# Kernel optimization log

Measured on AMD Instinct MI355X. Metric: run time of the kernel, lower is better.

Reference implementation:

```python
import jax, jax.numpy as jnp
import numpy as np

MASK_VALUE = float(-2**32 + 1)  # additive fill used by the torch module
B, QT, KT, D = 16, 2048, 2048, 1024


def setup_inputs() -> dict:
    key = jax.random.key(0)
    kq, kk, kv, kql, kkl = jax.random.split(key, 5)
    return {
        "Q": jax.random.normal(kq, (B, QT, D), dtype=jnp.float32),
        "K": jax.random.normal(kk, (B, KT, D), dtype=jnp.float32),
        "V": jax.random.normal(kv, (B, KT, D), dtype=jnp.float32),
        "Q_lengths": jax.random.randint(kql, (B,), 1, QT + 1, dtype=jnp.int32),
        "K_lengths": jax.random.randint(kkl, (B,), 1, KT + 1, dtype=jnp.int32),
    }


def reference(Q, K, V, Q_lengths, K_lengths):
    # dot-product scores: [b, qt, kt]
    logits = jnp.einsum("bqd,bkd->bqk", Q, K)
    # length mask: outer product of row-valid and col-valid masks
    q_valid = (jnp.arange(Q.shape[1]) < Q_lengths[:, None]).astype(logits.dtype)  # [b, qt]
    k_valid = (jnp.arange(K.shape[1]) < K_lengths[:, None]).astype(logits.dtype)  # [b, kt]
    mask = q_valid[:, :, None] * k_valid[:, None, :]                               # [b, qt, kt]
    logits = mask * logits + (1.0 - mask) * MASK_VALUE
    attention = jax.nn.softmax(logits, axis=-1)
    return jnp.einsum("bqk,bkd->bqd", attention, V)
```

## Files before the change

### kernel.cpp

```cpp
#include <hip/hip_runtime.h>

#define BATCH 16
#define QT    2048
#define KTOT  2048
#define DIM   1024
#define NITEMS (BATCH * (QT / 32))

typedef __attribute__((ext_vector_type(8))) _Float16 f16x8;
typedef __attribute__((ext_vector_type(4))) _Float16 f16x4;
typedef __attribute__((ext_vector_type(2))) _Float16 f16x2;
typedef __attribute__((ext_vector_type(4))) float    f32x4;

__global__ __launch_bounds__(256) void conv_k(const float* __restrict__ K,
                                              _Float16* __restrict__ Kf) {
    const size_t idx = ((size_t)blockIdx.x * 256 + threadIdx.x) * 8;
    f32x4 a0 = *(const f32x4*)(K + idx);
    f32x4 a1 = *(const f32x4*)(K + idx + 4);
    f16x8 h;
#pragma unroll
    for (int j = 0; j < 4; ++j) { h[j] = (_Float16)a0[j]; h[4 + j] = (_Float16)a1[j]; }
    *(f16x8*)(Kf + idx) = h;
}

__global__ __launch_bounds__(256) void trans_v(const float* __restrict__ V,
                                               _Float16* __restrict__ Vt) {
    const int blk = blockIdx.x;
    const int b   = blk >> 9;
    const int kt0 = ((blk >> 4) & 31) << 6;
    const int d0  = (blk & 15) << 6;
    __shared__ _Float16 tbuf[64][65];
    const int tid = threadIdx.x;
    const int cr  = tid >> 4;
    const int c4  = (tid & 15) << 2;
#pragma unroll
    for (int p = 0; p < 4; ++p) {
        const int r = cr + p * 16;
        f32x4 v = *(const f32x4*)(V + ((size_t)(b * KTOT + kt0 + r)) * DIM + d0 + c4);
#pragma unroll
        for (int j = 0; j < 4; ++j) tbuf[r][c4 + j] = (_Float16)v[j];
    }
    __syncthreads();
#pragma unroll
    for (int p = 0; p < 4; ++p) {
        const int dr = cr + p * 16;
        f16x4 o;
#pragma unroll
        for (int j = 0; j < 4; ++j) o[j] = tbuf[c4 + j][dr];
        *(f16x4*)(Vt + ((size_t)(b * DIM + d0 + dr)) * KTOT + kt0 + c4) = o;
    }
}

__global__ __launch_bounds__(64) void fill_mean_vt(const _Float16* __restrict__ Vt,
                                                   const int* __restrict__ Qlen,
                                                   float* __restrict__ out) {
    const int row = blockIdx.x * 64 + threadIdx.x;
    const int b = row >> 10, d = row & 1023;
    const f16x8* src = (const f16x8*)(Vt + (size_t)row * KTOT);
    float s = 0.0f;
    for (int i = 0; i < KTOT / 8; ++i) {
        f16x8 v = src[i];
#pragma unroll
        for (int j = 0; j < 8; ++j) s += (float)v[j];
    }
    const float mv = s * (1.0f / (float)KTOT);
    const int qlen = Qlen[b];
    for (int q = qlen; q < QT; ++q)
        out[((size_t)(b * QT + q)) * DIM + d] = mv;
}

__global__ __launch_bounds__(512, 2) void attn_main(
    const float* __restrict__ Q, const int* __restrict__ Qlen, const int* __restrict__ Klen,
    const _Float16* __restrict__ Kf, const _Float16* __restrict__ Vt,
    float* __restrict__ out, unsigned* __restrict__ counter) {

    __shared__ float    sred[2][8][32][33];
    __shared__ _Float16 pbuf[2][32][40];
    __shared__ float    arow[2][32];
    __shared__ float    lrow[32];
    __shared__ unsigned item_s;

    const int tid  = threadIdx.x;
    const int w    = tid >> 6;
    const int ln   = tid & 63;
    const int l16  = ln & 15;
    const int quad = ln >> 4;
    const int d0   = w << 7;
    const int sr  = tid >> 4;
    const int scg = tid & 15;

    for (;;) {
        __syncthreads();
        if (tid == 0) item_s = atomicAdd(counter, 1u);
        __syncthreads();
        const unsigned item = item_s;
        if (item >= NITEMS) break;
        const int b    = item >> 6;
        const int qt   = (item & 63) << 5;
        const int qlen = Qlen[b];
        if (qt >= qlen) continue;
        const int klen = Klen[b];
        const int nkt  = (klen + 31) >> 5;

        f16x8 qh[2][4], ql[2][4];
#pragma unroll
        for (int mi = 0; mi < 2; ++mi)
#pragma unroll
            for (int kc = 0; kc < 4; ++kc) {
                const float* src = Q + ((size_t)(b * QT + qt + mi * 16 + l16)) * DIM
                                     + d0 + kc * 32 + quad * 8;
                f32x4 a0 = *(const f32x4*)src;
                f32x4 a1 = *(const f32x4*)(src + 4);
                f16x8 h, l;
#pragma unroll
                for (int j = 0; j < 4; ++j) {
                    _Float16 h0 = (_Float16)a0[j];
                    h[j] = h0; l[j] = (_Float16)(a0[j] - (float)h0);
                    _Float16 h1 = (_Float16)a1[j];
                    h[4 + j] = h1; l[4 + j] = (_Float16)(a1[j] - (float)h1);
                }
                qh[mi][kc] = h; ql[mi][kc] = l;
            }

        f32x4 o[2][8];
        const f32x4 fzero = {0.0f, 0.0f, 0.0f, 0.0f};
#pragma unroll
        for (int mi = 0; mi < 2; ++mi)
#pragma unroll
            for (int nd = 0; nd < 8; ++nd) o[mi][nd] = fzero;

        float msx = -3.0e38f, lsx = 0.0f;

        f16x8 kf[2][4];
        {
            const _Float16* kb = Kf + ((size_t)(b * KTOT + l16)) * DIM + d0 + quad * 8;
#pragma unroll
            for (int ni = 0; ni < 2; ++ni)
#pragma unroll
                for (int kc = 0; kc < 4; ++kc)
                    kf[ni][kc] = *(const f16x8*)(kb + (size_t)(ni * 16) * DIM + kc * 32);
        }

        f16x8 vf[8];

        for (int t = 0; t <= nkt; ++t) {
            const int cur = t & 1, prv = cur ^ 1;

            if (t < nkt) {
                f32x4 s[2][2];
                s[0][0] = fzero; s[0][1] = fzero; s[1][0] = fzero; s[1][1] = fzero;
#pragma unroll
                for (int kc = 0; kc < 4; ++kc)
#pragma unroll
                    for (int ni = 0; ni < 2; ++ni) {
                        s[0][ni] = __builtin_amdgcn_mfma_f32_16x16x32_f16(qh[0][kc], kf[ni][kc], s[0][ni], 0, 0, 0);
                        s[1][ni] = __builtin_amdgcn_mfma_f32_16x16x32_f16(qh[1][kc], kf[ni][kc], s[1][ni], 0, 0, 0);
                        s[0][ni] = __builtin_amdgcn_mfma_f32_16x16x32_f16(ql[0][kc], kf[ni][kc], s[0][ni], 0, 0, 0);
                        s[1][ni] = __builtin_amdgcn_mfma_f32_16x16x32_f16(ql[1][kc], kf[ni][kc], s[1][ni], 0, 0, 0);
                    }
#pragma unroll
                for (int mi = 0; mi < 2; ++mi)
#pragma unroll
                    for (int ni = 0; ni < 2; ++ni)
#pragma unroll
                        for (int r2 = 0; r2 < 4; ++r2)
                            sred[cur][w][mi * 16 + quad * 4 + r2][ni * 16 + l16] = s[mi][ni][r2];
            }

            if (t > 0) {
                const int kt0p = (t - 1) << 5;
                const int c0 = scg * 2, c1 = c0 + 1;
                float x0 = 0.0f, x1 = 0.0f;
#pragma unroll
                for (int ww = 0; ww < 8; ++ww) {
                    x0 += sred[prv][ww][sr][c0];
                    x1 += sred[prv][ww][sr][c1];
                }
                if (kt0p + c0 >= klen) x0 = -3.0e38f;
                if (kt0p + c1 >= klen) x1 = -3.0e38f;
                float pm = fmaxf(x0, x1);
#pragma unroll
                for (int off = 1; off < 16; off <<= 1) pm = fmaxf(pm, __shfl_xor(pm, off, 64));
                const float mn    = fmaxf(msx, pm);
                const float alpha = __expf(msx - mn);
                const float p0 = __expf(x0 - mn), p1 = __expf(x1 - mn);
                float ps = p0 + p1;
#pragma unroll
                for (int off = 1; off < 16; off <<= 1) ps += __shfl_xor(ps, off, 64);
                lsx = lsx * alpha + ps;
                msx = mn;
                f16x2 pw; pw[0] = (_Float16)p0; pw[1] = (_Float16)p1;
                *(f16x2*)&pbuf[prv][sr][c0] = pw;
                if (scg == 0) arow[prv][sr] = alpha;
            }

            if (t + 1 < nkt) {
                const int ktn = (t + 1) << 5;
                const _Float16* kb = Kf + ((size_t)(b * KTOT + ktn + l16)) * DIM
                                        + d0 + quad * 8;
#pragma unroll
                for (int ni = 0; ni < 2; ++ni)
#pragma unroll
                    for (int kc = 0; kc < 4; ++kc)
                        kf[ni][kc] = *(const f16x8*)(kb + (size_t)(ni * 16) * DIM + kc * 32);
            }

            __syncthreads();

            if (t > 0) {
                f32x4 av0 = *(const f32x4*)&arow[prv][quad * 4];
                f32x4 av1 = *(const f32x4*)&arow[prv][16 + quad * 4];
#pragma unroll
                for (int nd = 0; nd < 8; ++nd) { o[0][nd] *= av0; o[1][nd] *= av1; }

                f16x8 pa[2];
#pragma unroll
                for (int mi = 0; mi < 2; ++mi)
                    pa[mi] = *(const f16x8*)&pbuf[prv][mi * 16 + l16][quad * 8];
#pragma unroll
                for (int nd = 0; nd < 8; ++nd) {
                    o[0][nd] = __builtin_amdgcn_mfma_f32_16x16x32_f16(pa[0], vf[nd], o[0][nd], 0, 0, 0);
                    o[1][nd] = __builtin_amdgcn_mfma_f32_16x16x32_f16(pa[1], vf[nd], o[1][nd], 0, 0, 0);
                }
            }

            if (t < nkt) {
                const int kt0 = t << 5;
#pragma unroll
                for (int nd = 0; nd < 8; ++nd)
                    vf[nd] = *(const f16x8*)(Vt + ((size_t)(b * DIM + d0 + nd * 16 + l16)) * KTOT
                                             + kt0 + quad * 8);
            }
        }

        if (scg == 0) lrow[sr] = lsx;
        __syncthreads();
        f32x4 li0, li1;
#pragma unroll
        for (int r2 = 0; r2 < 4; ++r2) {
            li0[r2] = 1.0f / lrow[quad * 4 + r2];
            li1[r2] = 1.0f / lrow[16 + quad * 4 + r2];
        }
#pragma unroll
        for (int mi = 0; mi < 2; ++mi)
#pragma unroll
            for (int r2 = 0; r2 < 4; ++r2) {
                const int row = qt + mi * 16 + quad * 4 + r2;
                if (row < qlen) {
                    const float inv = mi ? li1[r2] : li0[r2];
#pragma unroll
                    for (int nd = 0; nd < 8; ++nd)
                        out[((size_t)(b * QT + row)) * DIM + d0 + nd * 16 + l16] =
                            o[mi][nd][r2] * inv;
                }
            }
    }
}

__global__ __launch_bounds__(256) void fill_mean_f32(const float* __restrict__ V,
                                                     const int* __restrict__ Qlen,
                                                     float* __restrict__ out) {
    const int b  = blockIdx.x >> 4;
    const int d0 = (blockIdx.x & 15) << 6;
    const int qlen = Qlen[b];
    const int tid = threadIdx.x;
    const int dc = d0 + (tid & 63);
    const int part = tid >> 6;
    __shared__ float red[4][64];
    __shared__ float mcol[64];
    float sm = 0.0f;
    for (int kt = part; kt < KTOT; kt += 4)
        sm += V[((size_t)(b * KTOT + kt)) * DIM + dc];
    red[part][tid & 63] = sm;
    __syncthreads();
    if (tid < 64)
        mcol[tid] = (red[0][tid] + red[1][tid] + red[2][tid] + red[3][tid]) * (1.0f / (float)KTOT);
    __syncthreads();
    const float mv = mcol[tid & 63];
    for (int q = qlen + part; q < QT; q += 4)
        out[((size_t)(b * QT + q)) * DIM + dc] = mv;
}

__global__ __launch_bounds__(512) void attn_naive(
    const float* __restrict__ Q, const float* __restrict__ K, const float* __restrict__ V,
    const int* __restrict__ Qlen, const int* __restrict__ Klen, float* __restrict__ out) {
    const int blk  = blockIdx.x;
    const int b    = blk >> 8;
    const int qb   = (blk & 255) << 3;
    const int qlen = Qlen[b];
    if (qb >= qlen) return;
    const int klen = Klen[b];
    const int tid  = threadIdx.x;
    const int wid  = tid >> 6, ln = tid & 63;
    const int q    = qb + wid;
    __shared__ float kbuf[1024], vbuf[1024];
    f32x4 qr[4];
#pragma unroll
    for (int i = 0; i < 4; ++i)
        qr[i] = *(const f32x4*)(Q + ((size_t)(b * QT + q)) * DIM + i * 256 + ln * 4);
    const f32x4 fzero = {0.0f, 0.0f, 0.0f, 0.0f};
    f32x4 acc[4] = {fzero, fzero, fzero, fzero};
    float m = -3.0e38f, l = 0.0f;
    for (int kt = 0; kt < klen; ++kt) {
        __syncthreads();
        if (tid < 256)
            *(f32x4*)&kbuf[tid * 4] = *(const f32x4*)(K + ((size_t)(b * KTOT + kt)) * DIM + tid * 4);
        else
            *(f32x4*)&vbuf[(tid - 256) * 4] =
                *(const f32x4*)(V + ((size_t)(b * KTOT + kt)) * DIM + (tid - 256) * 4);
        __syncthreads();
        float sp = 0.0f;
#pragma unroll
        for (int i = 0; i < 4; ++i) {
            f32x4 kv = *(const f32x4*)&kbuf[i * 256 + ln * 4];
            sp += qr[i][0] * kv[0] + qr[i][1] * kv[1] + qr[i][2] * kv[2] + qr[i][3] * kv[3];
        }
#pragma unroll
        for (int off = 1; off < 64; off <<= 1) sp += __shfl_xor(sp, off, 64);
        const float mn = fmaxf(m, sp);
        const float a  = __expf(m - mn);
        const float p  = __expf(sp - mn);
        l = l * a + p; m = mn;
#pragma unroll
        for (int i = 0; i < 4; ++i) {
            f32x4 vv = *(const f32x4*)&vbuf[i * 256 + ln * 4];
            acc[i] = acc[i] * a + vv * p;
        }
    }
    if (q < qlen) {
        const float inv = 1.0f / l;
#pragma unroll
        for (int i = 0; i < 4; ++i)
            *(f32x4*)(out + ((size_t)(b * QT + q)) * DIM + i * 256 + ln * 4) = acc[i] * inv;
    }
}

extern "C" void kernel_launch(void* const* d_in, const int* in_sizes, int n_in,
                              void* d_out, int out_size, void* d_ws, size_t ws_size,
                              hipStream_t stream) {
    (void)in_sizes; (void)n_in; (void)out_size;
    const float* Q    = (const float*)d_in[0];
    const float* K    = (const float*)d_in[1];
    const float* V    = (const float*)d_in[2];
    const int*   Qlen = (const int*)d_in[3];
    const int*   Klen = (const int*)d_in[4];
    float*       out  = (float*)d_out;

    const size_t HALF = (size_t)BATCH * KTOT * DIM;
    const size_t NEED = HALF * 2  * sizeof(_Float16) + 64;
    if (ws_size >= NEED) {
        _Float16* kf = (_Float16*)d_ws;
        _Float16* vt = kf + HALF;
        unsigned* ctr = (unsigned*)((char*)d_ws + HALF * 2 * sizeof(_Float16));
        hipMemsetAsync(ctr, 0, sizeof(unsigned), stream);
        conv_k<<<dim3(16384), dim3(256), 0, stream>>>(K, kf);
        trans_v<<<dim3(8192), dim3(256), 0, stream>>>(V, vt);
        fill_mean_vt<<<dim3((BATCH * DIM) / 64), dim3(64), 0, stream>>>(vt, Qlen, out);
        attn_main<<<dim3(512), dim3(512), 0, stream>>>(Q, Qlen, Klen, kf, vt, out, ctr);
    } else {
        fill_mean_f32<<<dim3(BATCH * 16), dim3(256), 0, stream>>>(V, Qlen, out);
        attn_naive<<<dim3(4096), dim3(512), 0, stream>>>(Q, K, V, Qlen, Klen, out);
    }
}
```

Measured before the change: 781.3 us.

## Double-buffer K fragments two tiles ahead and parallelize mean fill kernel

The main attention loop is unrolled by two with two K register buffers, so each K tile is loaded two iterations before use instead of one, giving more latency hiding at the cost of extra registers. The score reduction buffer row is padded to 34 so pairs of scores can be read as float2. The fill-mean kernel splits each row sum across four threads with shuffle reduction and strides the output writes, and the persistent attention grid is halved to 256 blocks. Higher register pressure could reduce occupancy, and the smaller grid may leave compute units idle.

```diff
diff --git a/kernel.cpp b/kernel.cpp
--- a/kernel.cpp
+++ b/kernel.cpp
@@ -10,6 +10,7 @@
 typedef __attribute__((ext_vector_type(4))) _Float16 f16x4;
 typedef __attribute__((ext_vector_type(2))) _Float16 f16x2;
 typedef __attribute__((ext_vector_type(4))) float    f32x4;
+typedef __attribute__((ext_vector_type(2))) float    f32x2;
 
 __global__ __launch_bounds__(256) void conv_k(const float* __restrict__ K,
                                               _Float16* __restrict__ Kf) {
@@ -50,21 +51,25 @@
     }
 }
 
-__global__ __launch_bounds__(64) void fill_mean_vt(const _Float16* __restrict__ Vt,
-                                                   const int* __restrict__ Qlen,
-                                                   float* __restrict__ out) {
-    const int row = blockIdx.x * 64 + threadIdx.x;
+__global__ __launch_bounds__(256) void fill_mean_vt(const _Float16* __restrict__ Vt,
+                                                    const int* __restrict__ Qlen,
+                                                    float* __restrict__ out) {
+    const int gid  = blockIdx.x * 256 + threadIdx.x;
+    const int row  = gid >> 2;
+    const int part = gid & 3;
     const int b = row >> 10, d = row & 1023;
-    const f16x8* src = (const f16x8*)(Vt + (size_t)row * KTOT);
+    const f16x8* src = (const f16x8*)(Vt + (size_t)row * KTOT) + part * (KTOT / 32);
     float s = 0.0f;
-    for (int i = 0; i < KTOT / 8; ++i) {
+    for (int i = 0; i < KTOT / 32; ++i) {
         f16x8 v = src[i];
 #pragma unroll
         for (int j = 0; j < 8; ++j) s += (float)v[j];
     }
+    s += __shfl_xor(s, 1, 64);
+    s += __shfl_xor(s, 2, 64);
     const float mv = s * (1.0f / (float)KTOT);
     const int qlen = Qlen[b];
-    for (int q = qlen; q < QT; ++q)
+    for (int q = qlen + part; q < QT; q += 4)
         out[((size_t)(b * QT + q)) * DIM + d] = mv;
 }
 
@@ -73,7 +78,7 @@
     const _Float16* __restrict__ Kf, const _Float16* __restrict__ Vt,
     float* __restrict__ out, unsigned* __restrict__ counter) {
 
-    __shared__ float    sred[2][8][32][33];
+    __shared__ float    sred[2][8][32][34];
     __shared__ _Float16 pbuf[2][32][40];
     __shared__ float    arow[2][32];
     __shared__ float    lrow[32];
@@ -130,107 +135,104 @@
 
         float msx = -3.0e38f, lsx = 0.0f;
 
-        f16x8 kf[2][4];
-        {
-            const _Float16* kb = Kf + ((size_t)(b * KTOT + l16)) * DIM + d0 + quad * 8;
-#pragma unroll
-            for (int ni = 0; ni < 2; ++ni)
-#pragma unroll
-                for (int kc = 0; kc < 4; ++kc)
-                    kf[ni][kc] = *(const f16x8*)(kb + (size_t)(ni * 16) * DIM + kc * 32);
-        }
-
+        f16x8 kfA[2][4], kfB[2][4];
         f16x8 vf[8];
 
-        for (int t = 0; t <= nkt; ++t) {
-            const int cur = t & 1, prv = cur ^ 1;
-
-            if (t < nkt) {
-                f32x4 s[2][2];
-                s[0][0] = fzero; s[0][1] = fzero; s[1][0] = fzero; s[1][1] = fzero;
-#pragma unroll
-                for (int kc = 0; kc < 4; ++kc)
-#pragma unroll
-                    for (int ni = 0; ni < 2; ++ni) {
-                        s[0][ni] = __builtin_amdgcn_mfma_f32_16x16x32_f16(qh[0][kc], kf[ni][kc], s[0][ni], 0, 0, 0);
-                        s[1][ni] = __builtin_amdgcn_mfma_f32_16x16x32_f16(qh[1][kc], kf[ni][kc], s[1][ni], 0, 0, 0);
-                        s[0][ni] = __builtin_amdgcn_mfma_f32_16x16x32_f16(ql[0][kc], kf[ni][kc], s[0][ni], 0, 0, 0);
-                        s[1][ni] = __builtin_amdgcn_mfma_f32_16x16x32_f16(ql[1][kc], kf[ni][kc], s[1][ni], 0, 0, 0);
-                    }
-#pragma unroll
-                for (int mi = 0; mi < 2; ++mi)
-#pragma unroll
-                    for (int ni = 0; ni < 2; ++ni)
-#pragma unroll
-                        for (int r2 = 0; r2 < 4; ++r2)
-                            sred[cur][w][mi * 16 + quad * 4 + r2][ni * 16 + l16] = s[mi][ni][r2];
-            }
-
-            if (t > 0) {
-                const int kt0p = (t - 1) << 5;
-                const int c0 = scg * 2, c1 = c0 + 1;
-                float x0 = 0.0f, x1 = 0.0f;
-#pragma unroll
-                for (int ww = 0; ww < 8; ++ww) {
-                    x0 += sred[prv][ww][sr][c0];
-                    x1 += sred[prv][ww][sr][c1];
-                }
-                if (kt0p + c0 >= klen) x0 = -3.0e38f;
-                if (kt0p + c1 >= klen) x1 = -3.0e38f;
-                float pm = fmaxf(x0, x1);
-#pragma unroll
-                for (int off = 1; off < 16; off <<= 1) pm = fmaxf(pm, __shfl_xor(pm, off, 64));
-                const float mn    = fmaxf(msx, pm);
-                const float alpha = __expf(msx - mn);
-                const float p0 = __expf(x0 - mn), p1 = __expf(x1 - mn);
-                float ps = p0 + p1;
-#pragma unroll
-                for (int off = 1; off < 16; off <<= 1) ps += __shfl_xor(ps, off, 64);
-                lsx = lsx * alpha + ps;
-                msx = mn;
-                f16x2 pw; pw[0] = (_Float16)p0; pw[1] = (_Float16)p1;
-                *(f16x2*)&pbuf[prv][sr][c0] = pw;
-                if (scg == 0) arow[prv][sr] = alpha;
-            }
-
-            if (t + 1 < nkt) {
-                const int ktn = (t + 1) << 5;
-                const _Float16* kb = Kf + ((size_t)(b * KTOT + ktn + l16)) * DIM
-                                        + d0 + quad * 8;
-#pragma unroll
-                for (int ni = 0; ni < 2; ++ni)
-#pragma unroll
-                    for (int kc = 0; kc < 4; ++kc)
-                        kf[ni][kc] = *(const f16x8*)(kb + (size_t)(ni * 16) * DIM + kc * 32);
-            }
-
-            __syncthreads();
-
-            if (t > 0) {
-                f32x4 av0 = *(const f32x4*)&arow[prv][quad * 4];
-                f32x4 av1 = *(const f32x4*)&arow[prv][16 + quad * 4];
-#pragma unroll
-                for (int nd = 0; nd < 8; ++nd) { o[0][nd] *= av0; o[1][nd] *= av1; }
-
-                f16x8 pa[2];
-#pragma unroll
-                for (int mi = 0; mi < 2; ++mi)
-                    pa[mi] = *(const f16x8*)&pbuf[prv][mi * 16 + l16][quad * 8];
-#pragma unroll
-                for (int nd = 0; nd < 8; ++nd) {
-                    o[0][nd] = __builtin_amdgcn_mfma_f32_16x16x32_f16(pa[0], vf[nd], o[0][nd], 0, 0, 0);
-                    o[1][nd] = __builtin_amdgcn_mfma_f32_16x16x32_f16(pa[1], vf[nd], o[1][nd], 0, 0, 0);
-                }
-            }
-
-            if (t < nkt) {
-                const int kt0 = t << 5;
-#pragma unroll
-                for (int nd = 0; nd < 8; ++nd)
-                    vf[nd] = *(const f16x8*)(Vt + ((size_t)(b * DIM + d0 + nd * 16 + l16)) * KTOT
-                                             + kt0 + quad * 8);
-            }
-        }
+#define KLOAD(DST, TT)                                                          \
+        {                                                                       \
+            const _Float16* kb_ = Kf + ((size_t)(b * KTOT + ((TT) << 5) + l16)) * DIM \
+                                     + d0 + quad * 8;                           \
+            _Pragma("unroll")                                                   \
+            for (int ni = 0; ni < 2; ++ni)                                      \
+                _Pragma("unroll")                                               \
+                for (int kc = 0; kc < 4; ++kc)                                  \
+                    DST[ni][kc] = *(const f16x8*)(kb_ + (size_t)(ni * 16) * DIM + kc * 32); \
+        }
+
+        KLOAD(kfA, 0);
+        if (nkt > 1) KLOAD(kfB, 1);
+
+#define TILE_BODY(T, KFU)                                                       \
+        {                                                                       \
+            const int t_ = (T);                                                 \
+            const int cur_ = t_ & 1, prv_ = cur_ ^ 1;                           \
+            if (t_ < nkt) {                                                     \
+                f32x4 s00 = fzero, s01 = fzero, s10 = fzero, s11 = fzero;       \
+                _Pragma("unroll")                                               \
+                for (int kc = 0; kc < 4; ++kc) {                                \
+                    s00 = __builtin_amdgcn_mfma_f32_16x16x32_f16(qh[0][kc], KFU[0][kc], s00, 0, 0, 0); \
+                    s10 = __builtin_amdgcn_mfma_f32_16x16x32_f16(qh[1][kc], KFU[0][kc], s10, 0, 0, 0); \
+                    s00 = __builtin_amdgcn_mfma_f32_16x16x32_f16(ql[0][kc], KFU[0][kc], s00, 0, 0, 0); \
+                    s10 = __builtin_amdgcn_mfma_f32_16x16x32_f16(ql[1][kc], KFU[0][kc], s10, 0, 0, 0); \
+                    s01 = __builtin_amdgcn_mfma_f32_16x16x32_f16(qh[0][kc], KFU[1][kc], s01, 0, 0, 0); \
+                    s11 = __builtin_amdgcn_mfma_f32_16x16x32_f16(qh[1][kc], KFU[1][kc], s11, 0, 0, 0); \
+                    s01 = __builtin_amdgcn_mfma_f32_16x16x32_f16(ql[0][kc], KFU[1][kc], s01, 0, 0, 0); \
+                    s11 = __builtin_amdgcn_mfma_f32_16x16x32_f16(ql[1][kc], KFU[1][kc], s11, 0, 0, 0); \
+                }                                                               \
+                _Pragma("unroll")                                               \
+                for (int r2 = 0; r2 < 4; ++r2) {                                \
+                    sred[cur_][w][quad * 4 + r2][l16]           = s00[r2];      \
+                    sred[cur_][w][quad * 4 + r2][16 + l16]      = s01[r2];      \
+                    sred[cur_][w][16 + quad * 4 + r2][l16]      = s10[r2];      \
+                    sred[cur_][w][16 + quad * 4 + r2][16 + l16] = s11[r2];      \
+                }                                                               \
+            }                                                                   \
+            if (t_ > 0) {                                                       \
+                const int kt0p = (t_ - 1) << 5;                                 \
+                const int c0 = scg * 2, c1 = c0 + 1;                            \
+                float x0 = 0.0f, x1 = 0.0f;                                     \
+                _Pragma("unroll")                                               \
+                for (int ww = 0; ww < 8; ++ww) {                                \
+                    f32x2 xp = *(const f32x2*)&sred[prv_][ww][sr][c0];          \
+                    x0 += xp[0]; x1 += xp[1];                                   \
+                }                                                               \
+                if (kt0p + c0 >= klen) x0 = -3.0e38f;                           \
+                if (kt0p + c1 >= klen) x1 = -3.0e38f;                           \
+                float pm = fmaxf(x0, x1);                                       \
+                _Pragma("unroll")                                               \
+                for (int off = 1; off < 16; off <<= 1) pm = fmaxf(pm, __shfl_xor(pm, off, 64)); \
+                const float mn    = fmaxf(msx, pm);                             \
+                const float alpha = __expf(msx - mn);                           \
+                const float p0 = __expf(x0 - mn), p1 = __expf(x1 - mn);         \
+                float ps = p0 + p1;                                             \
+                _Pragma("unroll")                                               \
+                for (int off = 1; off < 16; off <<= 1) ps += __shfl_xor(ps, off, 64); \
+                lsx = lsx * alpha + ps;                                         \
+                msx = mn;                                                       \
+                f16x2 pw; pw[0] = (_Float16)p0; pw[1] = (_Float16)p1;           \
+                *(f16x2*)&pbuf[prv_][sr][c0] = pw;                              \
+                if (scg == 0) arow[prv_][sr] = alpha;                           \
+            }                                                                   \
+            if (t_ + 2 < nkt) KLOAD(KFU, t_ + 2);                               \
+            __syncthreads();                                                    \
+            if (t_ > 0) {                                                       \
+                f32x4 av0 = *(const f32x4*)&arow[prv_][quad * 4];               \
+                f32x4 av1 = *(const f32x4*)&arow[prv_][16 + quad * 4];          \
+                _Pragma("unroll")                                               \
+                for (int nd = 0; nd < 8; ++nd) { o[0][nd] *= av0; o[1][nd] *= av1; } \
+                f16x8 pa0 = *(const f16x8*)&pbuf[prv_][l16][quad * 8];          \
+                f16x8 pa1 = *(const f16x8*)&pbuf[prv_][16 + l16][quad * 8];     \
+                _Pragma("unroll")                                               \
+                for (int nd = 0; nd < 8; ++nd) {                                \
+                    o[0][nd] = __builtin_amdgcn_mfma_f32_16x16x32_f16(pa0, vf[nd], o[0][nd], 0, 0, 0); \
+                    o[1][nd] = __builtin_amdgcn_mfma_f32_16x16x32_f16(pa1, vf[nd], o[1][nd], 0, 0, 0); \
+                }                                                               \
+            }                                                                   \
+            if (t_ < nkt) {                                                     \
+                const int kt0v = t_ << 5;                                       \
+                _Pragma("unroll")                                               \
+                for (int nd = 0; nd < 8; ++nd)                                  \
+                    vf[nd] = *(const f16x8*)(Vt + ((size_t)(b * DIM + d0 + nd * 16 + l16)) * KTOT \
+                                             + kt0v + quad * 8);                \
+            }                                                                   \
+        }
+
+        for (int t = 0; t <= nkt; t += 2) {
+            TILE_BODY(t, kfA);
+            if (t + 1 <= nkt) TILE_BODY(t + 1, kfB);
+        }
+#undef TILE_BODY
+#undef KLOAD
 
         if (scg == 0) lrow[sr] = lsx;
         __syncthreads();
@@ -354,8 +356,8 @@
         hipMemsetAsync(ctr, 0, sizeof(unsigned), stream);
         conv_k<<<dim3(16384), dim3(256), 0, stream>>>(K, kf);
         trans_v<<<dim3(8192), dim3(256), 0, stream>>>(V, vt);
-        fill_mean_vt<<<dim3((BATCH * DIM) / 64), dim3(64), 0, stream>>>(vt, Qlen, out);
-        attn_main<<<dim3(512), dim3(512), 0, stream>>>(Q, Qlen, Klen, kf, vt, out, ctr);
+        fill_mean_vt<<<dim3(256), dim3(256), 0, stream>>>(vt, Qlen, out);
+        attn_main<<<dim3(256), dim3(512), 0, stream>>>(Q, Qlen, Klen, kf, vt, out, ctr);
     } else {
         fill_mean_f32<<<dim3(BATCH * 16), dim3(256), 0, stream>>>(V, Qlen, out);
         attn_naive<<<dim3(4096), dim3(512), 0, stream>>>(Q, K, V, Qlen, Klen, out);
```

After: 955.4 us. 1.22x slower.

## Use XCD-local work queues, split mean-fill rows, and pad score buffer

Applied to the files above, without the earlier changes.

Replaces the single global work counter with eight per-XCD counters. Each counter covers two batches, so blocks on one XCD share K/V in their local L2, and a block steals from other queues once its own is empty. The persistent grid drops from 512 to 256 blocks. The mean-fill kernel now splits each row across four threads joined by shuffles, and the score reduction buffer is padded to 34 so it can be read as float2 pairs. The smaller grid may cut occupancy, and the queue-stealing path adds extra atomics.

```diff
diff --git a/kernel.cpp b/kernel.cpp
--- a/kernel.cpp
+++ b/kernel.cpp
@@ -10,6 +10,7 @@
 typedef __attribute__((ext_vector_type(4))) _Float16 f16x4;
 typedef __attribute__((ext_vector_type(2))) _Float16 f16x2;
 typedef __attribute__((ext_vector_type(4))) float    f32x4;
+typedef __attribute__((ext_vector_type(2))) float    f32x2;
 
 __global__ __launch_bounds__(256) void conv_k(const float* __restrict__ K,
                                               _Float16* __restrict__ Kf) {
@@ -50,21 +51,25 @@
     }
 }
 
-__global__ __launch_bounds__(64) void fill_mean_vt(const _Float16* __restrict__ Vt,
-                                                   const int* __restrict__ Qlen,
-                                                   float* __restrict__ out) {
-    const int row = blockIdx.x * 64 + threadIdx.x;
+__global__ __launch_bounds__(256) void fill_mean_vt(const _Float16* __restrict__ Vt,
+                                                    const int* __restrict__ Qlen,
+                                                    float* __restrict__ out) {
+    const int gid  = blockIdx.x * 256 + threadIdx.x;
+    const int row  = gid >> 2;
+    const int part = gid & 3;
     const int b = row >> 10, d = row & 1023;
-    const f16x8* src = (const f16x8*)(Vt + (size_t)row * KTOT);
+    const f16x8* src = (const f16x8*)(Vt + (size_t)row * KTOT) + part * (KTOT / 32);
     float s = 0.0f;
-    for (int i = 0; i < KTOT / 8; ++i) {
+    for (int i = 0; i < KTOT / 32; ++i) {
         f16x8 v = src[i];
 #pragma unroll
         for (int j = 0; j < 8; ++j) s += (float)v[j];
     }
+    s += __shfl_xor(s, 1, 64);
+    s += __shfl_xor(s, 2, 64);
     const float mv = s * (1.0f / (float)KTOT);
     const int qlen = Qlen[b];
-    for (int q = qlen; q < QT; ++q)
+    for (int q = qlen + part; q < QT; q += 4)
         out[((size_t)(b * QT + q)) * DIM + d] = mv;
 }
 
@@ -73,7 +78,7 @@
     const _Float16* __restrict__ Kf, const _Float16* __restrict__ Vt,
     float* __restrict__ out, unsigned* __restrict__ counter) {
 
-    __shared__ float    sred[2][8][32][33];
+    __shared__ float    sred[2][8][32][34];
     __shared__ _Float16 pbuf[2][32][40];
     __shared__ float    arow[2][32];
     __shared__ float    lrow[32];
@@ -88,14 +93,29 @@
     const int sr  = tid >> 4;
     const int scg = tid & 15;
 
+    const unsigned bxcd = (unsigned)(blockIdx.x & 7);
+    unsigned gx = bxcd;
+    int goff = 0;
+
     for (;;) {
         __syncthreads();
-        if (tid == 0) item_s = atomicAdd(counter, 1u);
+        if (tid == 0) {
+            unsigned pick = 0xFFFFFFFFu;
+            while (goff < 8) {
+                unsigned it = atomicAdd(&counter[gx], 1u);
+                if (it < 128u) { pick = gx * 128u + it; break; }
+                ++goff;
+                gx = (bxcd + (unsigned)goff) & 7u;
+            }
+            item_s = pick;
+        }
         __syncthreads();
         const unsigned item = item_s;
-        if (item >= NITEMS) break;
-        const int b    = item >> 6;
-        const int qt   = (item & 63) << 5;
+        if (item == 0xFFFFFFFFu) break;
+        const int grp  = (int)(item >> 7);
+        const int ii   = (int)(item & 127u);
+        const int b    = (grp << 1) + (ii >> 6);
+        const int qt   = (ii & 63) << 5;
         const int qlen = Qlen[b];
         if (qt >= qlen) continue;
         const int klen = Klen[b];
@@ -146,24 +166,25 @@
             const int cur = t & 1, prv = cur ^ 1;
 
             if (t < nkt) {
-                f32x4 s[2][2];
-                s[0][0] = fzero; s[0][1] = fzero; s[1][0] = fzero; s[1][1] = fzero;
-#pragma unroll
-                for (int kc = 0; kc < 4; ++kc)
-#pragma unroll
-                    for (int ni = 0; ni < 2; ++ni) {
-                        s[0][ni] = __builtin_amdgcn_mfma_f32_16x16x32_f16(qh[0][kc], kf[ni][kc], s[0][ni], 0, 0, 0);
-                        s[1][ni] = __builtin_amdgcn_mfma_f32_16x16x32_f16(qh[1][kc], kf[ni][kc], s[1][ni], 0, 0, 0);
-                        s[0][ni] = __builtin_amdgcn_mfma_f32_16x16x32_f16(ql[0][kc], kf[ni][kc], s[0][ni], 0, 0, 0);
-                        s[1][ni] = __builtin_amdgcn_mfma_f32_16x16x32_f16(ql[1][kc], kf[ni][kc], s[1][ni], 0, 0, 0);
-                    }
-#pragma unroll
-                for (int mi = 0; mi < 2; ++mi)
-#pragma unroll
-                    for (int ni = 0; ni < 2; ++ni)
-#pragma unroll
-                        for (int r2 = 0; r2 < 4; ++r2)
-                            sred[cur][w][mi * 16 + quad * 4 + r2][ni * 16 + l16] = s[mi][ni][r2];
+                f32x4 s00 = fzero, s01 = fzero, s10 = fzero, s11 = fzero;
+#pragma unroll
+                for (int kc = 0; kc < 4; ++kc) {
+                    s00 = __builtin_amdgcn_mfma_f32_16x16x32_f16(qh[0][kc], kf[0][kc], s00, 0, 0, 0);
+                    s10 = __builtin_amdgcn_mfma_f32_16x16x32_f16(qh[1][kc], kf[0][kc], s10, 0, 0, 0);
+                    s00 = __builtin_amdgcn_mfma_f32_16x16x32_f16(ql[0][kc], kf[0][kc], s00, 0, 0, 0);
+                    s10 = __builtin_amdgcn_mfma_f32_16x16x32_f16(ql[1][kc], kf[0][kc], s10, 0, 0, 0);
+                    s01 = __builtin_amdgcn_mfma_f32_16x16x32_f16(qh[0][kc], kf[1][kc], s01, 0, 0, 0);
+                    s11 = __builtin_amdgcn_mfma_f32_16x16x32_f16(qh[1][kc], kf[1][kc], s11, 0, 0, 0);
+                    s01 = __builtin_amdgcn_mfma_f32_16x16x32_f16(ql[0][kc], kf[1][kc], s01, 0, 0, 0);
+                    s11 = __builtin_amdgcn_mfma_f32_16x16x32_f16(ql[1][kc], kf[1][kc], s11, 0, 0, 0);
+                }
+#pragma unroll
+                for (int r2 = 0; r2 < 4; ++r2) {
+                    sred[cur][w][quad * 4 + r2][l16]           = s00[r2];
+                    sred[cur][w][quad * 4 + r2][16 + l16]      = s01[r2];
+                    sred[cur][w][16 + quad * 4 + r2][l16]      = s10[r2];
+                    sred[cur][w][16 + quad * 4 + r2][16 + l16] = s11[r2];
+                }
             }
 
             if (t > 0) {
@@ -172,8 +193,8 @@
                 float x0 = 0.0f, x1 = 0.0f;
 #pragma unroll
                 for (int ww = 0; ww < 8; ++ww) {
-                    x0 += sred[prv][ww][sr][c0];
-                    x1 += sred[prv][ww][sr][c1];
+                    f32x2 xp = *(const f32x2*)&sred[prv][ww][sr][c0];
+                    x0 += xp[0]; x1 += xp[1];
                 }
                 if (kt0p + c0 >= klen) x0 = -3.0e38f;
                 if (kt0p + c1 >= klen) x1 = -3.0e38f;
@@ -212,23 +233,21 @@
 #pragma unroll
                 for (int nd = 0; nd < 8; ++nd) { o[0][nd] *= av0; o[1][nd] *= av1; }
 
-                f16x8 pa[2];
-#pragma unroll
-                for (int mi = 0; mi < 2; ++mi)
-                    pa[mi] = *(const f16x8*)&pbuf[prv][mi * 16 + l16][quad * 8];
+                f16x8 pa0 = *(const f16x8*)&pbuf[prv][l16][quad * 8];
+                f16x8 pa1 = *(const f16x8*)&pbuf[prv][16 + l16][quad * 8];
 #pragma unroll
                 for (int nd = 0; nd < 8; ++nd) {
-                    o[0][nd] = __builtin_amdgcn_mfma_f32_16x16x32_f16(pa[0], vf[nd], o[0][nd], 0, 0, 0);
-                    o[1][nd] = __builtin_amdgcn_mfma_f32_16x16x32_f16(pa[1], vf[nd], o[1][nd], 0, 0, 0);
+                    o[0][nd] = __builtin_amdgcn_mfma_f32_16x16x32_f16(pa0, vf[nd], o[0][nd], 0, 0, 0);
+                    o[1][nd] = __builtin_amdgcn_mfma_f32_16x16x32_f16(pa1, vf[nd], o[1][nd], 0, 0, 0);
                 }
             }
 
             if (t < nkt) {
-                const int kt0 = t << 5;
+                const int kt0v = t << 5;
 #pragma unroll
                 for (int nd = 0; nd < 8; ++nd)
                     vf[nd] = *(const f16x8*)(Vt + ((size_t)(b * DIM + d0 + nd * 16 + l16)) * KTOT
-                                             + kt0 + quad * 8);
+                                             + kt0v + quad * 8);
             }
         }
 
@@ -351,11 +370,11 @@
         _Float16* kf = (_Float16*)d_ws;
         _Float16* vt = kf + HALF;
         unsigned* ctr = (unsigned*)((char*)d_ws + HALF * 2 * sizeof(_Float16));
-        hipMemsetAsync(ctr, 0, sizeof(unsigned), stream);
+        hipMemsetAsync(ctr, 0, 8 * sizeof(unsigned), stream);
         conv_k<<<dim3(16384), dim3(256), 0, stream>>>(K, kf);
         trans_v<<<dim3(8192), dim3(256), 0, stream>>>(V, vt);
-        fill_mean_vt<<<dim3((BATCH * DIM) / 64), dim3(64), 0, stream>>>(vt, Qlen, out);
-        attn_main<<<dim3(512), dim3(512), 0, stream>>>(Q, Qlen, Klen, kf, vt, out, ctr);
+        fill_mean_vt<<<dim3(256), dim3(256), 0, stream>>>(vt, Qlen, out);
+        attn_main<<<dim3(256), dim3(512), 0, stream>>>(Q, Qlen, Klen, kf, vt, out, ctr);
     } else {
         fill_mean_f32<<<dim3(BATCH * 16), dim3(256), 0, stream>>>(V, Qlen, out);
         attn_naive<<<dim3(4096), dim3(512), 0, stream>>>(Q, K, V, Qlen, Klen, out);
```

Result: faster. 740.6 us (-5.2%).
